# Kernel optimization log

Measured on AMD Instinct MI355X. Metric: run time of the kernel, lower is better.

Reference implementation:

```python
import jax, jax.numpy as jnp
import numpy as np
from jax import lax

EPS = 1e-5  # BatchNorm eps (eval mode, running stats)
HEADS = 8

# --- surrogate-gradient Heaviside (sigmoid surrogate, alpha=4) ---
@jax.custom_vjp
def spike(u):
    return (u >= 0.0).astype(u.dtype)

def _spike_fwd(u):
    return spike(u), u

def _spike_bwd(u, g):
    s = jax.nn.sigmoid(4.0 * u)
    return (g * 4.0 * s * (1.0 - s),)

spike.defvjp(_spike_fwd, _spike_bwd)

def lif(x, tau=0.5, threshold=1.0):
    """Multi-step LIF over leading time axis: v_t = tau*v_{t-1} + x_t,
    s_t = H(v_t - threshold), hard reset v_t *= (1 - s_t)."""
    def step(v, xt):
        v = tau * v + xt
        s = spike(v - threshold)
        return v * (1.0 - s), s
    _, out = lax.scan(step, jnp.zeros_like(x[0]), x)
    return out

def bn_eval(x, gamma, beta, mean, var):
    # x: (T,B,C,N); per-channel affine using running stats
    inv = gamma / jnp.sqrt(var + EPS)
    return x * inv[None, None, :, None] + (beta - mean * inv)[None, None, :, None]

def setup_inputs() -> dict:
    key = jax.random.key(0)
    ks = jax.random.split(key, 12)
    T, B, C, H, W = 4, 32, 384, 16, 16
    d = {}
    d['x'] = jax.random.normal(ks[0], (T, B, C, H, W), dtype=jnp.float32)
    # 1x1 Conv1d weights == (C_out, C_in) matrices
    sc = 1.0 / np.sqrt(C)
    d['q_w'] = jax.random.normal(ks[1], (C, C), dtype=jnp.float32) * sc
    d['q_gamma'] = jnp.ones((C,), jnp.float32)
    d['q_beta'] = jnp.zeros((C,), jnp.float32)
    d['q_mean'] = jax.random.normal(ks[2], (C,), dtype=jnp.float32) * 0.1
    d['q_var'] = jax.random.uniform(ks[3], (C,), dtype=jnp.float32) + 0.5
    d['k_w'] = jax.random.normal(ks[4], (C, C), dtype=jnp.float32) * sc
    d['k_gamma'] = jnp.ones((C,), jnp.float32)
    d['k_beta'] = jnp.zeros((C,), jnp.float32)
    d['k_mean'] = jax.random.normal(ks[5], (C,), dtype=jnp.float32) * 0.1
    d['k_var'] = jax.random.uniform(ks[6], (C,), dtype=jnp.float32) + 0.5
    d['proj_w'] = jax.random.normal(ks[7], (C, C), dtype=jnp.float32) * sc
    d['proj_b'] = jax.random.normal(ks[8], (C,), dtype=jnp.float32) * 0.01
    d['proj_gamma'] = jnp.ones((C,), jnp.float32)
    d['proj_beta'] = jnp.zeros((C,), jnp.float32)
    d['proj_mean'] = jax.random.normal(ks[9], (C,), dtype=jnp.float32) * 0.1
    d['proj_var'] = jax.random.uniform(ks[10], (C,), dtype=jnp.float32) + 0.5
    d['mem_alpha'] = jnp.float32(0.2)
    return d

def reference(x, q_w, q_gamma, q_beta, q_mean, q_var,
              k_w, k_gamma, k_beta, k_mean, k_var,
              proj_w, proj_b, proj_gamma, proj_beta, proj_mean, proj_var,
              mem_alpha):
    T, B, C, H, W = x.shape
    Hh = HEADS
    Dh = C // Hh
    N = H * W
    # proj_lif applied to raw input, then flatten spatial dims
    s = lif(x, tau=0.5, threshold=1.0).reshape(T, B, C, N)
    # q path: 1x1 conv (channel GEMM) -> BN -> LIF
    q = lif(bn_eval(jnp.einsum('tbcn,dc->tbdn', s, q_w), q_gamma, q_beta, q_mean, q_var),
            tau=0.5, threshold=1.0).reshape(T, B, Hh, Dh, N)
    # k path
    k = lif(bn_eval(jnp.einsum('tbcn,dc->tbdn', s, k_w), k_gamma, k_beta, k_mean, k_var),
            tau=0.5, threshold=1.0).reshape(T, B, Hh, Dh, N)
    # temporal decayed memory: m_0 = q_0; m_t = alpha*m_{t-1} + (1-alpha)*q_{t-1}
    def mstep(m_prev, q_prev):
        m = mem_alpha * m_prev + (1.0 - mem_alpha) * q_prev
        return m, m
    _, mems_rest = lax.scan(mstep, q[0], q[:-1])
    mems = jnp.concatenate([q[:1], mems_rest], axis=0)  # (T,B,Hh,Dh,N)
    # cat along Dh then sum == sum(mems)+sum(q)
    q_sum = jnp.sum(mems, axis=3, keepdims=True) + jnp.sum(q, axis=3, keepdims=True)
    attn = lif(q_sum, tau=0.5, threshold=0.5)  # (T,B,Hh,1,N)
    y = (attn * k).reshape(T, B, C, N)
    # proj conv (with bias) -> BN -> reshape back to (T,B,C,H,W)
    y = jnp.einsum('tbcn,dc->tbdn', y, proj_w) + proj_b[None, None, :, None]
    y = bn_eval(y, proj_gamma, proj_beta, proj_mean, proj_var)
    return y.reshape(T, B, C, H, W)
```

## Files before the change

### kernel.cpp

```cpp
#include <hip/hip_runtime.h>

#define T_ 4
#define B_ 32
#define C_ 384
#define N_ 256
#define HEADS_ 8
#define DH_ 48
#define EPS_ 1e-5f

typedef _Float16 f16;
typedef __attribute__((ext_vector_type(8))) _Float16 f16x8;
typedef __attribute__((ext_vector_type(16))) float f32x16;

#define PSCALE     4096.0f
#define PSCALE_INV (1.0f/4096.0f)

__global__ __launch_bounds__(256)
void wsplit_kernel(const float* __restrict__ qw, const float* __restrict__ kw,
                   const float* __restrict__ pw,
                   f16* __restrict__ q2, f16* __restrict__ k2, f16* __restrict__ p2)
{
    int i = blockIdx.x * 256 + threadIdx.x;
    if (i >= C_ * C_) return;
    const int NW = C_ * C_;
    {
        float w = qw[i]; f16 a = (f16)w; f16 b = (f16)((w - (float)a) * PSCALE);
        q2[i] = a; q2[NW + i] = b;
    }
    {
        float w = kw[i]; f16 a = (f16)w; f16 b = (f16)((w - (float)a) * PSCALE);
        k2[i] = a; k2[NW + i] = b;
    }
    {
        float w = pw[i]; f16 a = (f16)w; f16 b = (f16)((w - (float)a) * PSCALE);
        p2[i] = a; p2[NW + i] = b;
    }
}

__global__ __launch_bounds__(256)
void lif_transpose_kernel(const float* __restrict__ x, f16* __restrict__ s)
{
    __shared__ f16 Ls[64][72];
    const int tid = threadIdx.x;
    const int n0 = blockIdx.x * 64;
    const int c0 = blockIdx.y * 64;
    const int b  = blockIdx.z;
    const int cl = tid >> 4;
    const int nl = (tid & 15) * 4;

    float v[4][4];
#pragma unroll
    for (int i = 0; i < 4; ++i)
#pragma unroll
        for (int j = 0; j < 4; ++j) v[i][j] = 0.f;

    for (int t = 0; t < T_; ++t) {
        const float* xt = x + (((size_t)t * B_ + b) * C_) * N_;
#pragma unroll
        for (int i = 0; i < 4; ++i) {
            int c = c0 + cl + 16 * i;
            float4 xv = *(const float4*)&xt[(size_t)c * N_ + n0 + nl];
            float xa[4] = {xv.x, xv.y, xv.z, xv.w};
#pragma unroll
            for (int j = 0; j < 4; ++j) {
                float vv = 0.5f * v[i][j] + xa[j];
                int sp = (vv >= 1.0f) ? 1 : 0;
                v[i][j] = sp ? 0.f : vv;
                Ls[nl + j][cl + 16 * i] = sp ? (f16)1.0f : (f16)0.0f;
            }
        }
        __syncthreads();
        {
            int r = tid >> 2, ch = (tid & 3) * 16;
            uint4 w0 = *(const uint4*)&Ls[r][ch];
            uint4 w1 = *(const uint4*)&Ls[r][ch + 8];
            f16* dst = s + (((size_t)t * B_ + b) * N_ + n0 + r) * (size_t)C_ + c0 + ch;
            *(uint4*)dst = w0;
            *(uint4*)(dst + 8) = w1;
        }
        __syncthreads();
    }
}

__global__ __launch_bounds__(256)
void qk_gemm_kernel(const f16* __restrict__ Wp,
                    const f16* __restrict__ S,
                    const float* __restrict__ gamma, const float* __restrict__ beta,
                    const float* __restrict__ mean,  const float* __restrict__ var,
                    f16* __restrict__ spk)
{
    __shared__ f16 As[64][72];
    __shared__ f16 Bs[2][64][72];

    const int tid  = threadIdx.x;
    const int lane = tid & 63;
    const int wave = tid >> 6;
    const int wn = wave & 1, wd = wave >> 1;
    const int n0 = blockIdx.x * 64;
    const int d0 = blockIdx.y * 64;
    const int b  = blockIdx.z;

    const int l31 = lane & 31;
    const int lhi = lane >> 5;
    const int dcol = d0 + wd * 32 + l31;

    const float inv = gamma[dcol] / sqrtf(var[dcol] + EPS_);
    const float add = beta[dcol] - mean[dcol] * inv;

    const int sr = tid >> 2;
    const int sc = (tid & 3) * 16;

    float v[16];
#pragma unroll
    for (int r = 0; r < 16; ++r) v[r] = 0.f;

    for (int t = 0; t < T_; ++t) {
        const f16* St = S + (((size_t)t * B_ + b) * N_) * (size_t)C_;
        f32x16 acc0, acc1;
#pragma unroll
        for (int r = 0; r < 16; ++r) { acc0[r] = 0.f; acc1[r] = 0.f; }

        for (int kc = 0; kc < C_; kc += 64) {
            __syncthreads();
            const f16* ga = St + (size_t)(n0 + sr) * C_ + kc + sc;
            *(uint4*)&As[sr][sc]     = *(const uint4*)ga;
            *(uint4*)&As[sr][sc + 8] = *(const uint4*)(ga + 8);
            const f16* gb0 = Wp + (size_t)(d0 + sr) * C_ + kc + sc;
            *(uint4*)&Bs[0][sr][sc]     = *(const uint4*)gb0;
            *(uint4*)&Bs[0][sr][sc + 8] = *(const uint4*)(gb0 + 8);
            const f16* gb1 = gb0 + (size_t)C_ * C_;
            *(uint4*)&Bs[1][sr][sc]     = *(const uint4*)gb1;
            *(uint4*)&Bs[1][sr][sc + 8] = *(const uint4*)(gb1 + 8);
            __syncthreads();
#pragma unroll
            for (int kk = 0; kk < 4; ++kk) {
                const int ko = kk * 16 + lhi * 8;
                f16x8 af = *(const f16x8*)&As[wn * 32 + l31][ko];
                f16x8 b0 = *(const f16x8*)&Bs[0][wd * 32 + l31][ko];
                f16x8 b1 = *(const f16x8*)&Bs[1][wd * 32 + l31][ko];
                acc0 = __builtin_amdgcn_mfma_f32_32x32x16_f16(af, b0, acc0, 0, 0, 0);
                acc1 = __builtin_amdgcn_mfma_f32_32x32x16_f16(af, b1, acc1, 0, 0, 0);
            }
        }
        f16* spt = spk + (((size_t)t * B_ + b) * N_) * (size_t)C_;
#pragma unroll
        for (int r = 0; r < 16; ++r) {
            int nrow = n0 + wn * 32 + (r & 3) + 8 * (r >> 2) + 4 * lhi;
            float val = acc0[r] + acc1[r] * PSCALE_INV;
            float bnv = val * inv + add;
            float vv = 0.5f * v[r] + bnv;
            int sp = (vv >= 1.0f) ? 1 : 0;
            v[r] = sp ? 0.f : vv;
            spt[(size_t)nrow * C_ + dcol] = sp ? (f16)1.0f : (f16)0.0f;
        }
    }
}

__global__ __launch_bounds__(256)
void head_sum_kernel(const f16* __restrict__ q_spk, float* __restrict__ Sq)
{
    int i = blockIdx.x * 256 + threadIdx.x;
    if (i >= T_ * B_ * HEADS_ * N_) return;
    int n  = i & (N_ - 1);
    int h  = (i >> 8) & (HEADS_ - 1);
    int tb = i >> 11;
    const uint4* p = (const uint4*)(q_spk + ((size_t)tb * N_ + n) * C_ + h * DH_);
    int cnt = 0;
#pragma unroll
    for (int j = 0; j < 6; ++j) {
        uint4 w = p[j];
        cnt += __popc(w.x & 0x04000400u) + __popc(w.y & 0x04000400u)
             + __popc(w.z & 0x04000400u) + __popc(w.w & 0x04000400u);
    }
    Sq[i] = (float)cnt;
}

__global__ __launch_bounds__(256)
void attn_kernel(const float* __restrict__ Sq, const float* __restrict__ alpha_p,
                 unsigned char* __restrict__ attn)
{
    int i = blockIdx.x * 256 + threadIdx.x;
    if (i >= B_ * HEADS_ * N_) return;
    const float alpha = alpha_p[0];
    const int stride = B_ * HEADS_ * N_;
    float M = 0.f, v = 0.f, Sprev = 0.f;
#pragma unroll
    for (int t = 0; t < T_; ++t) {
        float Sqt = Sq[(size_t)t * stride + i];
        if (t == 0) M = Sqt;
        else        M = alpha * M + (1.f - alpha) * Sprev;
        float qsum = M + Sqt;
        float vv = 0.5f * v + qsum;
        unsigned char sp = (vv >= 0.5f) ? 1 : 0;
        v = sp ? 0.f : vv;
        attn[(size_t)t * stride + i] = sp;
        Sprev = Sqt;
    }
}

__global__ __launch_bounds__(256)
void proj_gemm_kernel(const f16* __restrict__ Wp,
                      const f16* __restrict__ K,
                      const unsigned char* __restrict__ attn,
                      const float* __restrict__ bias,
                      const float* __restrict__ gamma, const float* __restrict__ beta,
                      const float* __restrict__ mean,  const float* __restrict__ var,
                      float* __restrict__ out)
{
    __shared__ f16 As[64][72];
    __shared__ f16 Bs[2][64][72];

    const int tid  = threadIdx.x;
    const int lane = tid & 63;
    const int wave = tid >> 6;
    const int wn = wave & 1, wd = wave >> 1;
    const int n0 = blockIdx.x * 64;
    const int d0 = blockIdx.y * 64;
    const int tb = blockIdx.z;

    const int l31 = lane & 31;
    const int lhi = lane >> 5;
    const int dcol = d0 + wd * 32 + l31;

    const float inv = gamma[dcol] / sqrtf(var[dcol] + EPS_);
    const float add = beta[dcol] - mean[dcol] * inv + bias[dcol] * inv;

    const int sr = tid >> 2;
    const int sc = (tid & 3) * 16;

    const f16* Kt = K + (size_t)tb * N_ * C_;
    const unsigned char* At = attn + (size_t)tb * HEADS_ * N_;

    f32x16 acc0, acc1;
#pragma unroll
    for (int r = 0; r < 16; ++r) { acc0[r] = 0.f; acc1[r] = 0.f; }

    for (int kc = 0; kc < C_; kc += 64) {
        __syncthreads();
        {
            int c = kc + sc;
            int h = c / DH_;
            unsigned char am = At[(size_t)h * N_ + n0 + sr];
            if (am) {
                const f16* ga = Kt + (size_t)(n0 + sr) * C_ + c;
                *(uint4*)&As[sr][sc]     = *(const uint4*)ga;
                *(uint4*)&As[sr][sc + 8] = *(const uint4*)(ga + 8);
            } else {
                uint4 z = make_uint4(0, 0, 0, 0);
                *(uint4*)&As[sr][sc]     = z;
                *(uint4*)&As[sr][sc + 8] = z;
            }
        }
        const f16* gb0 = Wp + (size_t)(d0 + sr) * C_ + kc + sc;
        *(uint4*)&Bs[0][sr][sc]     = *(const uint4*)gb0;
        *(uint4*)&Bs[0][sr][sc + 8] = *(const uint4*)(gb0 + 8);
        const f16* gb1 = gb0 + (size_t)C_ * C_;
        *(uint4*)&Bs[1][sr][sc]     = *(const uint4*)gb1;
        *(uint4*)&Bs[1][sr][sc + 8] = *(const uint4*)(gb1 + 8);
        __syncthreads();
#pragma unroll
        for (int kk = 0; kk < 4; ++kk) {
            const int ko = kk * 16 + lhi * 8;
            f16x8 af = *(const f16x8*)&As[wn * 32 + l31][ko];
            f16x8 b0 = *(const f16x8*)&Bs[0][wd * 32 + l31][ko];
            f16x8 b1 = *(const f16x8*)&Bs[1][wd * 32 + l31][ko];
            acc0 = __builtin_amdgcn_mfma_f32_32x32x16_f16(af, b0, acc0, 0, 0, 0);
            acc1 = __builtin_amdgcn_mfma_f32_32x32x16_f16(af, b1, acc1, 0, 0, 0);
        }
    }
    float* orow = out + ((size_t)tb * C_ + dcol) * N_ + n0 + wn * 32 + 4 * lhi;
#pragma unroll
    for (int g = 0; g < 4; ++g) {
        float4 o;
        float v0 = acc0[g * 4 + 0] + acc1[g * 4 + 0] * PSCALE_INV;
        float v1 = acc0[g * 4 + 1] + acc1[g * 4 + 1] * PSCALE_INV;
        float v2 = acc0[g * 4 + 2] + acc1[g * 4 + 2] * PSCALE_INV;
        float v3 = acc0[g * 4 + 3] + acc1[g * 4 + 3] * PSCALE_INV;
        o.x = v0 * inv + add;
        o.y = v1 * inv + add;
        o.z = v2 * inv + add;
        o.w = v3 * inv + add;
        *(float4*)&orow[8 * g] = o;
    }
}

extern "C" void kernel_launch(void* const* d_in, const int* in_sizes, int n_in,
                              void* d_out, int out_size, void* d_ws, size_t ws_size,
                              hipStream_t stream)
{
    const float* x       = (const float*)d_in[0];
    const float* q_w     = (const float*)d_in[1];
    const float* q_gamma = (const float*)d_in[2];
    const float* q_beta  = (const float*)d_in[3];
    const float* q_mean  = (const float*)d_in[4];
    const float* q_var   = (const float*)d_in[5];
    const float* k_w     = (const float*)d_in[6];
    const float* k_gamma = (const float*)d_in[7];
    const float* k_beta  = (const float*)d_in[8];
    const float* k_mean  = (const float*)d_in[9];
    const float* k_var   = (const float*)d_in[10];
    const float* proj_w  = (const float*)d_in[11];
    const float* proj_b  = (const float*)d_in[12];
    const float* p_gamma = (const float*)d_in[13];
    const float* p_beta  = (const float*)d_in[14];
    const float* p_mean  = (const float*)d_in[15];
    const float* p_var   = (const float*)d_in[16];
    const float* m_alpha = (const float*)d_in[17];

    float* out = (float*)d_out;

    const size_t SPK_BYTES = (size_t)T_ * B_ * N_ * C_ * sizeof(f16);
    const size_t W2_BYTES  = (size_t)2 * C_ * C_ * sizeof(f16);
    const size_t SQ_BYTES  = (size_t)T_ * B_ * HEADS_ * N_ * sizeof(float);

    unsigned char* ws = (unsigned char*)d_ws;
    size_t off = 0;
    auto carve = [&](size_t bytes) {
        off = (off + 255) & ~(size_t)255;
        void* p = ws + off;
        off += bytes;
        return p;
    };
    f16* s_f16  = (f16*)carve(SPK_BYTES);
    f16* q_spk  = (f16*)carve(SPK_BYTES);
    f16* k_spk  = (f16*)carve(SPK_BYTES);
    f16* Wq2    = (f16*)carve(W2_BYTES);
    f16* Wk2    = (f16*)carve(W2_BYTES);
    f16* Wp2    = (f16*)carve(W2_BYTES);
    float* Sq   = (float*)carve(SQ_BYTES);
    unsigned char* attn = (unsigned char*)carve((size_t)T_ * B_ * HEADS_ * N_);

    wsplit_kernel<<<(C_ * C_ + 255) / 256, 256, 0, stream>>>(q_w, k_w, proj_w, Wq2, Wk2, Wp2);

    dim3 lgrid(N_ / 64, C_ / 64, B_);
    lif_transpose_kernel<<<lgrid, 256, 0, stream>>>(x, s_f16);

    dim3 ggrid(N_ / 64, C_ / 64, B_);
    qk_gemm_kernel<<<ggrid, 256, 0, stream>>>(Wq2, s_f16, q_gamma, q_beta, q_mean, q_var, q_spk);
    qk_gemm_kernel<<<ggrid, 256, 0, stream>>>(Wk2, s_f16, k_gamma, k_beta, k_mean, k_var, k_spk);

    head_sum_kernel<<<(T_ * B_ * HEADS_ * N_ + 255) / 256, 256, 0, stream>>>(q_spk, Sq);

    attn_kernel<<<(B_ * HEADS_ * N_ + 255) / 256, 256, 0, stream>>>(Sq, m_alpha, attn);

    dim3 pgrid(N_ / 64, C_ / 64, T_ * B_);
    proj_gemm_kernel<<<pgrid, 256, 0, stream>>>(Wp2, k_spk, attn, proj_b,
                                                p_gamma, p_beta, p_mean, p_var, out);
}
```

Before: 243.7 us.

## Fuse Q/K GEMMs, merge prep and head-sum kernels, retile projection GEMM

```diff
diff --git a/kernel.cpp b/kernel.cpp
--- a/kernel.cpp
+++ b/kernel.cpp
@@ -7,6 +7,7 @@
 #define HEADS_ 8
 #define DH_ 48
 #define EPS_ 1e-5f
+#define NW_ (C_*C_)
 
 typedef _Float16 f16;
 typedef __attribute__((ext_vector_type(8))) _Float16 f16x8;
@@ -16,31 +17,33 @@
 #define PSCALE_INV (1.0f/4096.0f)
 
 __global__ __launch_bounds__(256)
-void wsplit_kernel(const float* __restrict__ qw, const float* __restrict__ kw,
-                   const float* __restrict__ pw,
-                   f16* __restrict__ q2, f16* __restrict__ k2, f16* __restrict__ p2)
-{
-    int i = blockIdx.x * 256 + threadIdx.x;
-    if (i >= C_ * C_) return;
-    const int NW = C_ * C_;
-    {
-        float w = qw[i]; f16 a = (f16)w; f16 b = (f16)((w - (float)a) * PSCALE);
-        q2[i] = a; q2[NW + i] = b;
-    }
-    {
-        float w = kw[i]; f16 a = (f16)w; f16 b = (f16)((w - (float)a) * PSCALE);
-        k2[i] = a; k2[NW + i] = b;
-    }
-    {
-        float w = pw[i]; f16 a = (f16)w; f16 b = (f16)((w - (float)a) * PSCALE);
-        p2[i] = a; p2[NW + i] = b;
-    }
-}
-
-__global__ __launch_bounds__(256)
-void lif_transpose_kernel(const float* __restrict__ x, f16* __restrict__ s)
+void prep_kernel(const float* __restrict__ x, f16* __restrict__ s,
+                 const float* __restrict__ qw, const float* __restrict__ kw,
+                 const float* __restrict__ pw,
+                 f16* __restrict__ q2, f16* __restrict__ k2, f16* __restrict__ p2)
 {
     __shared__ f16 Ls[64][72];
+    if (blockIdx.z == 32) {
+        int idx = (blockIdx.y * 4 + blockIdx.x) * 256 + threadIdx.x;
+#pragma unroll
+        for (int it = 0; it < 24; ++it) {
+            {
+                float w = qw[idx]; f16 a = (f16)w; f16 bb = (f16)((w - (float)a) * PSCALE);
+                q2[idx] = a; q2[NW_ + idx] = bb;
+            }
+            {
+                float w = kw[idx]; f16 a = (f16)w; f16 bb = (f16)((w - (float)a) * PSCALE);
+                k2[idx] = a; k2[NW_ + idx] = bb;
+            }
+            {
+                float w = pw[idx]; f16 a = (f16)w; f16 bb = (f16)((w - (float)a) * PSCALE);
+                p2[idx] = a; p2[NW_ + idx] = bb;
+            }
+            idx += 6144;
+        }
+        return;
+    }
+
     const int tid = threadIdx.x;
     const int n0 = blockIdx.x * 64;
     const int c0 = blockIdx.y * 64;
@@ -82,111 +85,130 @@
     }
 }
 
-__global__ __launch_bounds__(256)
-void qk_gemm_kernel(const f16* __restrict__ Wp,
-                    const f16* __restrict__ S,
-                    const float* __restrict__ gamma, const float* __restrict__ beta,
-                    const float* __restrict__ mean,  const float* __restrict__ var,
-                    f16* __restrict__ spk)
+__global__ __launch_bounds__(128, 2)
+void qk_fused_kernel(const f16* __restrict__ Wq, const f16* __restrict__ Wk,
+                     const f16* __restrict__ S,
+                     const float* __restrict__ qg, const float* __restrict__ qb,
+                     const float* __restrict__ qm, const float* __restrict__ qv,
+                     const float* __restrict__ kg, const float* __restrict__ kb,
+                     const float* __restrict__ km, const float* __restrict__ kv,
+                     f16* __restrict__ q_spk, f16* __restrict__ k_spk)
 {
     __shared__ f16 As[64][72];
-    __shared__ f16 Bs[2][64][72];
+    __shared__ f16 Bs[4][32][72];
 
     const int tid  = threadIdx.x;
     const int lane = tid & 63;
     const int wave = tid >> 6;
-    const int wn = wave & 1, wd = wave >> 1;
+    const int l31  = lane & 31;
+    const int lhi  = lane >> 5;
     const int n0 = blockIdx.x * 64;
-    const int d0 = blockIdx.y * 64;
+    const int d0 = blockIdx.y * 32;
     const int b  = blockIdx.z;
-
-    const int l31 = lane & 31;
-    const int lhi = lane >> 5;
-    const int dcol = d0 + wd * 32 + l31;
-
-    const float inv = gamma[dcol] / sqrtf(var[dcol] + EPS_);
-    const float add = beta[dcol] - mean[dcol] * inv;
-
-    const int sr = tid >> 2;
-    const int sc = (tid & 3) * 16;
-
-    float v[16];
-#pragma unroll
-    for (int r = 0; r < 16; ++r) v[r] = 0.f;
+    const int dcol = d0 + l31;
+
+    const float* g_  = wave ? kg : qg;
+    const float* be_ = wave ? kb : qb;
+    const float* m_  = wave ? km : qm;
+    const float* va_ = wave ? kv : qv;
+    f16* spk = wave ? k_spk : q_spk;
+
+    const float inv = g_[dcol] / sqrtf(va_[dcol] + EPS_);
+    const float add = be_[dcol] - m_[dcol] * inv;
+
+    const int ar = tid >> 1;
+    const int ac = (tid & 1) * 32;
+    const int br = tid >> 2;
+    const int bc = (tid & 3) * 16;
+
+    const f16* Bsrc0 = Wq;
+    const f16* Bsrc1 = Wq + NW_;
+    const f16* Bsrc2 = Wk;
+    const f16* Bsrc3 = Wk + NW_;
+
+    float v[32];
+#pragma unroll
+    for (int r = 0; r < 32; ++r) v[r] = 0.f;
 
     for (int t = 0; t < T_; ++t) {
-        const f16* St = S + (((size_t)t * B_ + b) * N_) * (size_t)C_;
-        f32x16 acc0, acc1;
-#pragma unroll
-        for (int r = 0; r < 16; ++r) { acc0[r] = 0.f; acc1[r] = 0.f; }
+        const f16* St = S + ((size_t)(t * B_ + b) * N_) * (size_t)C_;
+        f32x16 acc0[2], acc1[2];
+#pragma unroll
+        for (int s2 = 0; s2 < 2; ++s2)
+#pragma unroll
+            for (int r = 0; r < 16; ++r) { acc0[s2][r] = 0.f; acc1[s2][r] = 0.f; }
 
         for (int kc = 0; kc < C_; kc += 64) {
             __syncthreads();
-            const f16* ga = St + (size_t)(n0 + sr) * C_ + kc + sc;
-            *(uint4*)&As[sr][sc]     = *(const uint4*)ga;
-            *(uint4*)&As[sr][sc + 8] = *(const uint4*)(ga + 8);
-            const f16* gb0 = Wp + (size_t)(d0 + sr) * C_ + kc + sc;
-            *(uint4*)&Bs[0][sr][sc]     = *(const uint4*)gb0;
-            *(uint4*)&Bs[0][sr][sc + 8] = *(const uint4*)(gb0 + 8);
-            const f16* gb1 = gb0 + (size_t)C_ * C_;
-            *(uint4*)&Bs[1][sr][sc]     = *(const uint4*)gb1;
-            *(uint4*)&Bs[1][sr][sc + 8] = *(const uint4*)(gb1 + 8);
+            const f16* ga = St + (size_t)(n0 + ar) * C_ + kc + ac;
+            *(uint4*)&As[ar][ac]      = *(const uint4*)(ga);
+            *(uint4*)&As[ar][ac + 8]  = *(const uint4*)(ga + 8);
+            *(uint4*)&As[ar][ac + 16] = *(const uint4*)(ga + 16);
+            *(uint4*)&As[ar][ac + 24] = *(const uint4*)(ga + 24);
+            {
+                size_t wo = (size_t)(d0 + br) * C_ + kc + bc;
+                *(uint4*)&Bs[0][br][bc]     = *(const uint4*)(Bsrc0 + wo);
+                *(uint4*)&Bs[0][br][bc + 8] = *(const uint4*)(Bsrc0 + wo + 8);
+                *(uint4*)&Bs[1][br][bc]     = *(const uint4*)(Bsrc1 + wo);
+                *(uint4*)&Bs[1][br][bc + 8] = *(const uint4*)(Bsrc1 + wo + 8);
+                *(uint4*)&Bs[2][br][bc]     = *(const uint4*)(Bsrc2 + wo);
+                *(uint4*)&Bs[2][br][bc + 8] = *(const uint4*)(Bsrc2 + wo + 8);
+                *(uint4*)&Bs[3][br][bc]     = *(const uint4*)(Bsrc3 + wo);
+                *(uint4*)&Bs[3][br][bc + 8] = *(const uint4*)(Bsrc3 + wo + 8);
+            }
             __syncthreads();
 #pragma unroll
             for (int kk = 0; kk < 4; ++kk) {
                 const int ko = kk * 16 + lhi * 8;
-                f16x8 af = *(const f16x8*)&As[wn * 32 + l31][ko];
-                f16x8 b0 = *(const f16x8*)&Bs[0][wd * 32 + l31][ko];
-                f16x8 b1 = *(const f16x8*)&Bs[1][wd * 32 + l31][ko];
-                acc0 = __builtin_amdgcn_mfma_f32_32x32x16_f16(af, b0, acc0, 0, 0, 0);
-                acc1 = __builtin_amdgcn_mfma_f32_32x32x16_f16(af, b1, acc1, 0, 0, 0);
-            }
-        }
-        f16* spt = spk + (((size_t)t * B_ + b) * N_) * (size_t)C_;
+                f16x8 a0 = *(const f16x8*)&As[l31][ko];
+                f16x8 a1 = *(const f16x8*)&As[32 + l31][ko];
+                f16x8 b0 = *(const f16x8*)&Bs[2 * wave][l31][ko];
+                f16x8 b1 = *(const f16x8*)&Bs[2 * wave + 1][l31][ko];
+                acc0[0] = __builtin_amdgcn_mfma_f32_32x32x16_f16(a0, b0, acc0[0], 0, 0, 0);
+                acc0[1] = __builtin_amdgcn_mfma_f32_32x32x16_f16(a1, b0, acc0[1], 0, 0, 0);
+                acc1[0] = __builtin_amdgcn_mfma_f32_32x32x16_f16(a0, b1, acc1[0], 0, 0, 0);
+                acc1[1] = __builtin_amdgcn_mfma_f32_32x32x16_f16(a1, b1, acc1[1], 0, 0, 0);
+            }
+        }
+        f16* spt = spk + ((size_t)(t * B_ + b) * N_) * (size_t)C_;
+#pragma unroll
+        for (int s2 = 0; s2 < 2; ++s2)
 #pragma unroll
         for (int r = 0; r < 16; ++r) {
-            int nrow = n0 + wn * 32 + (r & 3) + 8 * (r >> 2) + 4 * lhi;
-            float val = acc0[r] + acc1[r] * PSCALE_INV;
+            int nrow = n0 + s2 * 32 + (r & 3) + 8 * (r >> 2) + 4 * lhi;
+            float val = acc0[s2][r] + acc1[s2][r] * PSCALE_INV;
             float bnv = val * inv + add;
-            float vv = 0.5f * v[r] + bnv;
+            float vv = 0.5f * v[s2 * 16 + r] + bnv;
             int sp = (vv >= 1.0f) ? 1 : 0;
-            v[r] = sp ? 0.f : vv;
+            v[s2 * 16 + r] = sp ? 0.f : vv;
             spt[(size_t)nrow * C_ + dcol] = sp ? (f16)1.0f : (f16)0.0f;
         }
     }
 }
 
 __global__ __launch_bounds__(256)
-void head_sum_kernel(const f16* __restrict__ q_spk, float* __restrict__ Sq)
+void head_attn_kernel(const f16* __restrict__ q_spk,
+                      const float* __restrict__ alpha_p,
+                      unsigned char* __restrict__ attn)
 {
     int i = blockIdx.x * 256 + threadIdx.x;
-    if (i >= T_ * B_ * HEADS_ * N_) return;
-    int n  = i & (N_ - 1);
-    int h  = (i >> 8) & (HEADS_ - 1);
-    int tb = i >> 11;
-    const uint4* p = (const uint4*)(q_spk + ((size_t)tb * N_ + n) * C_ + h * DH_);
-    int cnt = 0;
-#pragma unroll
-    for (int j = 0; j < 6; ++j) {
-        uint4 w = p[j];
-        cnt += __popc(w.x & 0x04000400u) + __popc(w.y & 0x04000400u)
-             + __popc(w.z & 0x04000400u) + __popc(w.w & 0x04000400u);
-    }
-    Sq[i] = (float)cnt;
-}
-
-__global__ __launch_bounds__(256)
-void attn_kernel(const float* __restrict__ Sq, const float* __restrict__ alpha_p,
-                 unsigned char* __restrict__ attn)
-{
-    int i = blockIdx.x * 256 + threadIdx.x;
-    if (i >= B_ * HEADS_ * N_) return;
+    int n = i & (N_ - 1);
+    int h = (i >> 8) & (HEADS_ - 1);
+    int b = i >> 11;
     const float alpha = alpha_p[0];
     const int stride = B_ * HEADS_ * N_;
     float M = 0.f, v = 0.f, Sprev = 0.f;
 #pragma unroll
     for (int t = 0; t < T_; ++t) {
-        float Sqt = Sq[(size_t)t * stride + i];
+        const uint4* p = (const uint4*)(q_spk + (((size_t)(t * B_ + b) * N_) + n) * C_ + h * DH_);
+        int cnt = 0;
+#pragma unroll
+        for (int j = 0; j < 6; ++j) {
+            uint4 w = p[j];
+            cnt += __popc(w.x & 0x04000400u) + __popc(w.y & 0x04000400u)
+                 + __popc(w.z & 0x04000400u) + __popc(w.w & 0x04000400u);
+        }
+        float Sqt = (float)cnt;
         if (t == 0) M = Sqt;
         else        M = alpha * M + (1.f - alpha) * Sprev;
         float qsum = M + Sqt;
@@ -198,7 +220,7 @@
     }
 }
 
-__global__ __launch_bounds__(256)
+__global__ __launch_bounds__(128, 2)
 void proj_gemm_kernel(const f16* __restrict__ Wp,
                       const f16* __restrict__ K,
                       const unsigned char* __restrict__ attn,
@@ -207,80 +229,103 @@
                       const float* __restrict__ mean,  const float* __restrict__ var,
                       float* __restrict__ out)
 {
-    __shared__ f16 As[64][72];
+    __shared__ f16 As[128][72];
     __shared__ f16 Bs[2][64][72];
 
     const int tid  = threadIdx.x;
     const int lane = tid & 63;
     const int wave = tid >> 6;
-    const int wn = wave & 1, wd = wave >> 1;
-    const int n0 = blockIdx.x * 64;
+    const int l31  = lane & 31;
+    const int lhi  = lane >> 5;
+    const int n0 = blockIdx.x * 128;
     const int d0 = blockIdx.y * 64;
     const int tb = blockIdx.z;
 
-    const int l31 = lane & 31;
-    const int lhi = lane >> 5;
-    const int dcol = d0 + wd * 32 + l31;
-
-    const float inv = gamma[dcol] / sqrtf(var[dcol] + EPS_);
-    const float add = beta[dcol] - mean[dcol] * inv + bias[dcol] * inv;
-
-    const int sr = tid >> 2;
-    const int sc = (tid & 3) * 16;
+    float inv[2], add[2];
+#pragma unroll
+    for (int u = 0; u < 2; ++u) {
+        int d = d0 + u * 32 + l31;
+        float iv = gamma[d] / sqrtf(var[d] + EPS_);
+        inv[u] = iv;
+        add[u] = beta[d] - mean[d] * iv + bias[d] * iv;
+    }
 
     const f16* Kt = K + (size_t)tb * N_ * C_;
     const unsigned char* At = attn + (size_t)tb * HEADS_ * N_;
 
-    f32x16 acc0, acc1;
-#pragma unroll
-    for (int r = 0; r < 16; ++r) { acc0[r] = 0.f; acc1[r] = 0.f; }
+    const int brow = tid >> 1;
+    const int bcol = (tid & 1) * 32;
+
+    f32x16 acc[2][2][2];
+#pragma unroll
+    for (int s2 = 0; s2 < 2; ++s2)
+#pragma unroll
+        for (int u = 0; u < 2; ++u)
+#pragma unroll
+            for (int p = 0; p < 2; ++p)
+#pragma unroll
+                for (int r = 0; r < 16; ++r) acc[s2][u][p][r] = 0.f;
 
     for (int kc = 0; kc < C_; kc += 64) {
         __syncthreads();
         {
-            int c = kc + sc;
-            int h = c / DH_;
-            unsigned char am = At[(size_t)h * N_ + n0 + sr];
-            if (am) {
-                const f16* ga = Kt + (size_t)(n0 + sr) * C_ + c;
-                *(uint4*)&As[sr][sc]     = *(const uint4*)ga;
-                *(uint4*)&As[sr][sc + 8] = *(const uint4*)(ga + 8);
-            } else {
-                uint4 z = make_uint4(0, 0, 0, 0);
-                *(uint4*)&As[sr][sc]     = z;
-                *(uint4*)&As[sr][sc + 8] = z;
-            }
-        }
-        const f16* gb0 = Wp + (size_t)(d0 + sr) * C_ + kc + sc;
-        *(uint4*)&Bs[0][sr][sc]     = *(const uint4*)gb0;
-        *(uint4*)&Bs[0][sr][sc + 8] = *(const uint4*)(gb0 + 8);
-        const f16* gb1 = gb0 + (size_t)C_ * C_;
-        *(uint4*)&Bs[1][sr][sc]     = *(const uint4*)gb1;
-        *(uint4*)&Bs[1][sr][sc + 8] = *(const uint4*)(gb1 + 8);
+            int nn = n0 + tid;
+            const f16* ga = Kt + (size_t)nn * C_ + kc;
+#pragma unroll
+            for (int j = 0; j < 8; ++j) {
+                int c = kc + 8 * j;
+                int h = c / DH_;
+                unsigned char am = At[(size_t)h * N_ + nn];
+                uint4 val = am ? *(const uint4*)(ga + 8 * j) : make_uint4(0u, 0u, 0u, 0u);
+                *(uint4*)&As[tid][8 * j] = val;
+            }
+        }
+        {
+            size_t wo = (size_t)(d0 + brow) * C_ + kc + bcol;
+            *(uint4*)&Bs[0][brow][bcol]      = *(const uint4*)(Wp + wo);
+            *(uint4*)&Bs[0][brow][bcol + 8]  = *(const uint4*)(Wp + wo + 8);
+            *(uint4*)&Bs[0][brow][bcol + 16] = *(const uint4*)(Wp + wo + 16);
+            *(uint4*)&Bs[0][brow][bcol + 24] = *(const uint4*)(Wp + wo + 24);
+            *(uint4*)&Bs[1][brow][bcol]      = *(const uint4*)(Wp + NW_ + wo);
+            *(uint4*)&Bs[1][brow][bcol + 8]  = *(const uint4*)(Wp + NW_ + wo + 8);
+            *(uint4*)&Bs[1][brow][bcol + 16] = *(const uint4*)(Wp + NW_ + wo + 16);
+            *(uint4*)&Bs[1][brow][bcol + 24] = *(const uint4*)(Wp + NW_ + wo + 24);
+        }
         __syncthreads();
 #pragma unroll
         for (int kk = 0; kk < 4; ++kk) {
             const int ko = kk * 16 + lhi * 8;
-            f16x8 af = *(const f16x8*)&As[wn * 32 + l31][ko];
-            f16x8 b0 = *(const f16x8*)&Bs[0][wd * 32 + l31][ko];
-            f16x8 b1 = *(const f16x8*)&Bs[1][wd * 32 + l31][ko];
-            acc0 = __builtin_amdgcn_mfma_f32_32x32x16_f16(af, b0, acc0, 0, 0, 0);
-            acc1 = __builtin_amdgcn_mfma_f32_32x32x16_f16(af, b1, acc1, 0, 0, 0);
-        }
-    }
-    float* orow = out + ((size_t)tb * C_ + dcol) * N_ + n0 + wn * 32 + 4 * lhi;
-#pragma unroll
-    for (int g = 0; g < 4; ++g) {
-        float4 o;
-        float v0 = acc0[g * 4 + 0] + acc1[g * 4 + 0] * PSCALE_INV;
-        float v1 = acc0[g * 4 + 1] + acc1[g * 4 + 1] * PSCALE_INV;
-        float v2 = acc0[g * 4 + 2] + acc1[g * 4 + 2] * PSCALE_INV;
-        float v3 = acc0[g * 4 + 3] + acc1[g * 4 + 3] * PSCALE_INV;
-        o.x = v0 * inv + add;
-        o.y = v1 * inv + add;
-        o.z = v2 * inv + add;
-        o.w = v3 * inv + add;
-        *(float4*)&orow[8 * g] = o;
+            f16x8 a0  = *(const f16x8*)&As[wave * 64 + l31][ko];
+            f16x8 a1  = *(const f16x8*)&As[wave * 64 + 32 + l31][ko];
+            f16x8 b00 = *(const f16x8*)&Bs[0][l31][ko];
+            f16x8 b01 = *(const f16x8*)&Bs[0][32 + l31][ko];
+            f16x8 b10 = *(const f16x8*)&Bs[1][l31][ko];
+            f16x8 b11 = *(const f16x8*)&Bs[1][32 + l31][ko];
+            acc[0][0][0] = __builtin_amdgcn_mfma_f32_32x32x16_f16(a0, b00, acc[0][0][0], 0, 0, 0);
+            acc[0][1][0] = __builtin_amdgcn_mfma_f32_32x32x16_f16(a0, b01, acc[0][1][0], 0, 0, 0);
+            acc[1][0][0] = __builtin_amdgcn_mfma_f32_32x32x16_f16(a1, b00, acc[1][0][0], 0, 0, 0);
+            acc[1][1][0] = __builtin_amdgcn_mfma_f32_32x32x16_f16(a1, b01, acc[1][1][0], 0, 0, 0);
+            acc[0][0][1] = __builtin_amdgcn_mfma_f32_32x32x16_f16(a0, b10, acc[0][0][1], 0, 0, 0);
+            acc[0][1][1] = __builtin_amdgcn_mfma_f32_32x32x16_f16(a0, b11, acc[0][1][1], 0, 0, 0);
+            acc[1][0][1] = __builtin_amdgcn_mfma_f32_32x32x16_f16(a1, b10, acc[1][0][1], 0, 0, 0);
+            acc[1][1][1] = __builtin_amdgcn_mfma_f32_32x32x16_f16(a1, b11, acc[1][1][1], 0, 0, 0);
+        }
+    }
+#pragma unroll
+    for (int s2 = 0; s2 < 2; ++s2)
+#pragma unroll
+    for (int u = 0; u < 2; ++u) {
+        int dcol = d0 + u * 32 + l31;
+        float* orow = out + ((size_t)tb * C_ + dcol) * N_ + n0 + wave * 64 + s2 * 32 + 4 * lhi;
+#pragma unroll
+        for (int g = 0; g < 4; ++g) {
+            float4 o;
+            o.x = (acc[s2][u][0][g * 4 + 0] + acc[s2][u][1][g * 4 + 0] * PSCALE_INV) * inv[u] + add[u];
+            o.y = (acc[s2][u][0][g * 4 + 1] + acc[s2][u][1][g * 4 + 1] * PSCALE_INV) * inv[u] + add[u];
+            o.z = (acc[s2][u][0][g * 4 + 2] + acc[s2][u][1][g * 4 + 2] * PSCALE_INV) * inv[u] + add[u];
+            o.w = (acc[s2][u][0][g * 4 + 3] + acc[s2][u][1][g * 4 + 3] * PSCALE_INV) * inv[u] + add[u];
+            *(float4*)&orow[8 * g] = o;
+        }
     }
 }
 
@@ -310,8 +355,7 @@
     float* out = (float*)d_out;
 
     const size_t SPK_BYTES = (size_t)T_ * B_ * N_ * C_ * sizeof(f16);
-    const size_t W2_BYTES  = (size_t)2 * C_ * C_ * sizeof(f16);
-    const size_t SQ_BYTES  = (size_t)T_ * B_ * HEADS_ * N_ * sizeof(float);
+    const size_t W2_BYTES  = (size_t)2 * NW_ * sizeof(f16);
 
     unsigned char* ws = (unsigned char*)d_ws;
     size_t off = 0;
@@ -327,23 +371,20 @@
     f16* Wq2    = (f16*)carve(W2_BYTES);
     f16* Wk2    = (f16*)carve(W2_BYTES);
     f16* Wp2    = (f16*)carve(W2_BYTES);
-    float* Sq   = (float*)carve(SQ_BYTES);
     unsigned char* attn = (unsigned char*)carve((size_t)T_ * B_ * HEADS_ * N_);
 
-    wsplit_kernel<<<(C_ * C_ + 255) / 256, 256, 0, stream>>>(q_w, k_w, proj_w, Wq2, Wk2, Wp2);
-
-    dim3 lgrid(N_ / 64, C_ / 64, B_);
-    lif_transpose_kernel<<<lgrid, 256, 0, stream>>>(x, s_f16);
-
-    dim3 ggrid(N_ / 64, C_ / 64, B_);
-    qk_gemm_kernel<<<ggrid, 256, 0, stream>>>(Wq2, s_f16, q_gamma, q_beta, q_mean, q_var, q_spk);
-    qk_gemm_kernel<<<ggrid, 256, 0, stream>>>(Wk2, s_f16, k_gamma, k_beta, k_mean, k_var, k_spk);
-
-    head_sum_kernel<<<(T_ * B_ * HEADS_ * N_ + 255) / 256, 256, 0, stream>>>(q_spk, Sq);
-
-    attn_kernel<<<(B_ * HEADS_ * N_ + 255) / 256, 256, 0, stream>>>(Sq, m_alpha, attn);
-
-    dim3 pgrid(N_ / 64, C_ / 64, T_ * B_);
-    proj_gemm_kernel<<<pgrid, 256, 0, stream>>>(Wp2, k_spk, attn, proj_b,
-                                                p_gamma, p_beta, p_mean, p_var, out);
-}
+    dim3 pgrid1(4, 6, 33);
+    prep_kernel<<<pgrid1, 256, 0, stream>>>(x, s_f16, q_w, k_w, proj_w, Wq2, Wk2, Wp2);
+
+    dim3 qkgrid(N_ / 64, C_ / 32, B_);
+    qk_fused_kernel<<<qkgrid, 128, 0, stream>>>(Wq2, Wk2, s_f16,
+                                                q_gamma, q_beta, q_mean, q_var,
+                                                k_gamma, k_beta, k_mean, k_var,
+                                                q_spk, k_spk);
+
+    head_attn_kernel<<<(B_ * HEADS_ * N_) / 256, 256, 0, stream>>>(q_spk, m_alpha, attn);
+
+    dim3 pjgrid(N_ / 128, C_ / 64, T_ * B_);
+    proj_gemm_kernel<<<pjgrid, 128, 0, stream>>>(Wp2, k_spk, attn, proj_b,
+                                                 p_gamma, p_beta, p_mean, p_var, out);
+}
```

Result: slower. 254.5 us (+4.5%).
